# Kernel optimization log

Measured on AMD Instinct MI355X. Metric: run time of the kernel, lower is better.

Reference implementation:

```python
import jax, jax.numpy as jnp
import numpy as np

B, S, D, H = 2, 2048, 1024, 16
HD = D // H  # 64
NEG = 1.0e9


def setup_inputs() -> dict:
    key = jax.random.key(0)
    ks = jax.random.split(key, 9)
    scale = 1.0 / np.sqrt(D)
    return {
        "q_in": jax.random.normal(ks[0], (B, S, D), jnp.float32),
        "k_in": jax.random.normal(ks[1], (B, S, D), jnp.float32),
        "v_in": jax.random.normal(ks[2], (B, S, D), jnp.float32),
        "Wq": jax.random.normal(ks[3], (D, D), jnp.float32) * scale,
        "bq": jnp.zeros((D,), jnp.float32),
        "Wk": jax.random.normal(ks[4], (D, D), jnp.float32) * scale,
        "bk": jnp.zeros((D,), jnp.float32),
        "Wv": jax.random.normal(ks[5], (D, D), jnp.float32) * scale,
        "bv": jnp.zeros((D,), jnp.float32),
        "Wo": jax.random.normal(ks[6], (D, D), jnp.float32) * scale,
        "bo": jnp.zeros((D,), jnp.float32),
    }


def _split_heads(x):
    # [B,S,D] -> [B,H,S,HD]
    return x.reshape(B, S, H, HD).transpose(0, 2, 1, 3)


def reference(q_in, k_in, v_in, Wq, bq, Wk, bk, Wv, bv, Wo, bo):
    q = _split_heads(q_in @ Wq + bq)
    k = _split_heads(k_in @ Wk + bk)
    v = _split_heads(v_in @ Wv + bv)
    # scaled dot-product attention with additive causal mask (use_causal_mask=True)
    scores = jnp.einsum("bhqd,bhkd->bhqk", q, k) / jnp.sqrt(jnp.float32(HD))
    causal = jnp.tril(jnp.ones((S, S), jnp.float32))  # band_part(ones, -1, 0)
    scores = scores + (causal - 1.0) * NEG
    weights = jax.nn.softmax(scores, axis=-1)
    attn = jnp.einsum("bhqk,bhkd->bhqd", weights, v)
    concat = attn.transpose(0, 2, 1, 3).reshape(B, S, D)
    return concat @ Wo + bo
```

## Files before the change

kernel.cpp:

```cpp
#include <hip/hip_runtime.h>

#define B_  2
#define S_  2048
#define D_  1024
#define H_  16
#define HD_ 64
#define MM  (B_ * S_)

typedef __bf16 bf16;
typedef __attribute__((ext_vector_type(8))) __bf16 bf16x8;
typedef __attribute__((ext_vector_type(4))) __bf16 bf16x4;
typedef __attribute__((ext_vector_type(4))) float  f32x4;

__device__ inline float exp2g(float x) { return __builtin_amdgcn_exp2f(x); }

__device__ inline bf16x8 load8(const bf16* p) { return *(const bf16x8*)p; }
__device__ inline bf16x8 load8(const float* p) {
  float4 a = *(const float4*)p;
  float4 b = *(const float4*)(p + 4);
  bf16x8 r;
  r[0] = (bf16)a.x; r[1] = (bf16)a.y; r[2] = (bf16)a.z; r[3] = (bf16)a.w;
  r[4] = (bf16)b.x; r[5] = (bf16)b.y; r[6] = (bf16)b.z; r[7] = (bf16)b.w;
  return r;
}

__device__ inline void gld16(void* lds, const void* g) {
  __builtin_amdgcn_global_load_lds(
      (const __attribute__((address_space(1))) unsigned int*)g,
      (__attribute__((address_space(3))) unsigned int*)lds, 16, 0, 0);
}

__device__ inline void barrier_lds() {
  asm volatile("s_waitcnt lgkmcnt(0)" ::: "memory");
  __builtin_amdgcn_s_barrier();
}

__global__ __launch_bounds__(256) void transpose_w(
    const float* __restrict__ W0, const float* __restrict__ W1,
    const float* __restrict__ W2, const float* __restrict__ W3,
    bf16* __restrict__ T0, bf16* __restrict__ T1,
    bf16* __restrict__ T2, bf16* __restrict__ T3,
    const float* __restrict__ X0, const float* __restrict__ X1,
    const float* __restrict__ X2,
    bf16* __restrict__ Y0, bf16* __restrict__ Y1, bf16* __restrict__ Y2) {
  const int z = blockIdx.z;
  if (z >= 4) {
    const int p = z - 4, t = p >> 2;
    const float* src = t == 0 ? X0 : t == 1 ? X1 : X2;
    bf16* dst = t == 0 ? Y0 : t == 1 ? Y1 : Y2;
    long base = ((long)(p & 3) << 20) +
                (long)(blockIdx.y * 32 + blockIdx.x) * 1024 + threadIdx.x * 4;
    float4 v = *(const float4*)&src[base];
    bf16x4 o4;
    o4[0] = (bf16)v.x; o4[1] = (bf16)v.y; o4[2] = (bf16)v.z; o4[3] = (bf16)v.w;
    *(bf16x4*)&dst[base] = o4;
    return;
  }
  __shared__ bf16 t[32][40];
  const float* in = z == 0 ? W0 : z == 1 ? W1 : z == 2 ? W2 : W3;
  bf16* out = z == 0 ? T0 : z == 1 ? T1 : z == 2 ? T2 : T3;
  const int tx = threadIdx.x & 31;
  const int ty = threadIdx.x >> 5;
  const int r0 = blockIdx.y * 32, c0 = blockIdx.x * 32;
#pragma unroll
  for (int j = 0; j < 32; j += 8)
    t[ty + j][tx] = (bf16)in[(long)(r0 + ty + j) * D_ + (c0 + tx)];
  __syncthreads();
#pragma unroll
  for (int j = 0; j < 32; j += 8)
    out[(long)(c0 + ty + j) * D_ + (r0 + tx)] = t[tx][ty + j];
}

__global__ __launch_bounds__(256) void transpose_v64(const bf16* __restrict__ V,
                                                     bf16* __restrict__ VT) {
  __shared__ bf16 t[64][72];
  const int tid = threadIdx.x;
  const int s0 = blockIdx.x * 64;
  const int bh = blockIdx.y;
  const int b = bh >> 4, h = bh & 15;
  const bf16* ip = V + (long)b * S_ * D_ + h * HD_;
  bf16* op = VT + (long)bh * HD_ * S_;
#pragma unroll
  for (int i = 0; i < 2; ++i) {
    int c = tid + i * 256;
    int r = c >> 3, cc = (c & 7) * 8;
    *(bf16x8*)&t[r][cc] = *(const bf16x8*)&ip[(long)(s0 + r) * D_ + cc];
  }
  __syncthreads();
#pragma unroll
  for (int i = 0; i < 2; ++i) {
    int c = tid + i * 256;
    int d = c >> 3, sc = (c & 7) * 8;
    bf16x8 v;
#pragma unroll
    for (int j = 0; j < 8; ++j) v[j] = t[sc + j][d];
    *(bf16x8*)&op[(long)d * S_ + s0 + sc] = v;
  }
}

template <typename AT, typename OT>
__global__ __launch_bounds__(256) void gemm_bt_dma(
    const AT* __restrict__ A0, const AT* __restrict__ A1, const AT* __restrict__ A2,
    const bf16* __restrict__ B0, const bf16* __restrict__ B1, const bf16* __restrict__ B2,
    const float* __restrict__ c0, const float* __restrict__ c1, const float* __restrict__ c2,
    OT* __restrict__ C0, OT* __restrict__ C1, OT* __restrict__ C2,
    int M, int N, int K) {
  __shared__ bf16 lA[2][128][32];
  __shared__ bf16 lB[2][128][32];
  const int z = blockIdx.z;
  const AT*    A    = z == 0 ? A0 : z == 1 ? A1 : A2;
  const bf16*  Bt   = z == 0 ? B0 : z == 1 ? B1 : B2;
  const float* bias = z == 0 ? c0 : z == 1 ? c1 : c2;
  OT*          C    = z == 0 ? C0 : z == 1 ? C1 : C2;

  const int tid = threadIdx.x;
  const int lane = tid & 63, wave = tid >> 6;
  const int quad = lane >> 4, l16 = lane & 15;
  const int id = blockIdx.x + (blockIdx.y << 3);
  const int nid = (id & 7) * 32 + (id >> 3);
  const int bm = (nid >> 3) * 128, bn = (nid & 7) * 128;
  const int wm = (wave >> 1) * 64, wn = (wave & 1) * 64;

  f32x4 acc[4][4] = {};
  const int NT = K >> 5;

#define STAGE_DMA(buf, t)                                                    \
  {                                                                          \
    const int k0 = (t) << 5;                                                 \
    _Pragma("unroll") for (int i = 0; i < 2; ++i) {                          \
      const int nbase = wave * 128 + i * 64;    \
      const int n = nbase + lane;                                            \
      const int row = n >> 2, kc = (n & 3) * 8;                              \
      gld16(&lB[buf][0][0] + (long)nbase * 8,                                \
            &Bt[(long)(bn + row) * K + k0 + kc]);                            \
      if constexpr (__is_same(AT, bf16))                                     \
        gld16(&lA[buf][0][0] + (long)nbase * 8,                              \
              &A[(long)(bm + row) * K + k0 + kc]);                           \
    }                                                                        \
    if constexpr (!__is_same(AT, bf16)) {                                    \
      _Pragma("unroll") for (int i = 0; i < 2; ++i) {                        \
        int cch = tid + i * 256;                                             \
        int row = cch >> 2, kc = (cch & 3) * 8;                              \
        *(bf16x8*)&lA[buf][row][kc] =                                        \
            load8(&A[(long)(bm + row) * K + k0 + kc]);                       \
      }                                                                      \
    }                                                                        \
  }

  STAGE_DMA(0, 0);
  __syncthreads();

  for (int t = 0; t < NT; ++t) {
    const int buf = t & 1;
    if (t + 1 < NT) STAGE_DMA(buf ^ 1, t + 1);
    bf16x8 af[4], bfr[4];
#pragma unroll
    for (int i = 0; i < 4; ++i) {
      af[i]  = *(const bf16x8*)&lA[buf][wm + i * 16 + l16][quad * 8];
      bfr[i] = *(const bf16x8*)&lB[buf][wn + i * 16 + l16][quad * 8];
    }
#pragma unroll
    for (int mi = 0; mi < 4; ++mi)
#pragma unroll
      for (int ni = 0; ni < 4; ++ni)
        acc[mi][ni] = __builtin_amdgcn_mfma_f32_16x16x32_bf16(
            af[mi], bfr[ni], acc[mi][ni], 0, 0, 0);
    __syncthreads();
  }
#undef STAGE_DMA

#pragma unroll
  for (int mi = 0; mi < 4; ++mi)
#pragma unroll
    for (int ni = 0; ni < 4; ++ni) {
      int col = bn + wn + ni * 16 + l16;
      float bv = bias[col];
#pragma unroll
      for (int r = 0; r < 4; ++r) {
        int row = bm + wm + mi * 16 + quad * 4 + r;
        C[(long)row * N + col] = (OT)(acc[mi][ni][r] + bv);
      }
    }
}

__global__ __launch_bounds__(256) void gemm_bt_64(const bf16* __restrict__ A,
                                                  const bf16* __restrict__ Bt,
                                                  const float* __restrict__ bias,
                                                  float* __restrict__ C,
                                                  int M, int N, int K) {
  __shared__ bf16 lA[2][128][32];
  __shared__ bf16 lB[2][64][32];
  const int tid = threadIdx.x;
  const int lane = tid & 63, wave = tid >> 6;
  const int quad = lane >> 4, l16 = lane & 15;
  const int id = blockIdx.x + (blockIdx.y << 4);
  const int nid = (id & 7) * 64 + (id >> 3);
  const int bm = (nid >> 4) * 128, bn = (nid & 15) * 64;
  const int wm = (wave >> 1) * 64, wn = (wave & 1) * 32;

  f32x4 acc[4][2] = {};
  const int NT = K >> 5;

#define STAGE64(buf, t)                                                      \
  {                                                                          \
    const int k0 = (t) << 5;                                                 \
    _Pragma("unroll") for (int i = 0; i < 2; ++i) {                          \
      const int nbase = wave * 128 + i * 64;                                 \
      const int n = nbase + lane;                                            \
      const int row = n >> 2, kc = (n & 3) * 8;                              \
      gld16(&lA[buf][0][0] + (long)nbase * 8,                                \
            &A[(long)(bm + row) * K + k0 + kc]);                             \
    }                                                                        \
    {                                                                        \
      const int nbase = wave * 64;                                           \
      const int n = nbase + lane;                                            \
      const int row = n >> 2, kc = (n & 3) * 8;                              \
      gld16(&lB[buf][0][0] + (long)nbase * 8,                                \
            &Bt[(long)(bn + row) * K + k0 + kc]);                            \
    }                                                                        \
  }

  STAGE64(0, 0);
  __syncthreads();

  for (int t = 0; t < NT; ++t) {
    const int buf = t & 1;
    if (t + 1 < NT) STAGE64(buf ^ 1, t + 1);
    bf16x8 af[4], bfr[2];
#pragma unroll
    for (int i = 0; i < 4; ++i)
      af[i] = *(const bf16x8*)&lA[buf][wm + i * 16 + l16][quad * 8];
#pragma unroll
    for (int i = 0; i < 2; ++i)
      bfr[i] = *(const bf16x8*)&lB[buf][wn + i * 16 + l16][quad * 8];
#pragma unroll
    for (int mi = 0; mi < 4; ++mi)
#pragma unroll
      for (int ni = 0; ni < 2; ++ni)
        acc[mi][ni] = __builtin_amdgcn_mfma_f32_16x16x32_bf16(
            af[mi], bfr[ni], acc[mi][ni], 0, 0, 0);
    __syncthreads();
  }
#undef STAGE64

#pragma unroll
  for (int mi = 0; mi < 4; ++mi)
#pragma unroll
    for (int ni = 0; ni < 2; ++ni) {
      int col = bn + wn + ni * 16 + l16;
      float bv = bias[col];
#pragma unroll
      for (int r = 0; r < 4; ++r) {
        int row = bm + wm + mi * 16 + quad * 4 + r;
        C[(long)row * N + col] = acc[mi][ni][r] + bv;
      }
    }
}

#define SCALE_LOG2E 0.1803368801111244f

__device__ inline void attn_step5(bool diag, int qloc, int quad, int l16,
                                  const bf16 (*lKb)[64], const bf16 (*lVb)[64],
                                  bf16 (*lpw)[72], const bf16x8* aq,
                                  f32x4* o, float& l_s) {
  const int sw = l16 & 7;
  f32x4 s[4];
  __builtin_amdgcn_s_setprio(1);
#pragma unroll
  for (int ni = 0; ni < 4; ++ni) {
    f32x4 a = {};
#pragma unroll
    for (int c = 0; c < 2; ++c) {
      bf16x8 kf = *(const bf16x8*)&lKb[ni * 16 + l16][((c * 4 + quad) ^ sw) * 8];
      a = __builtin_amdgcn_mfma_f32_16x16x32_bf16(kf, aq[c], a, 0, 0, 0);
    }
    s[ni] = a * SCALE_LOG2E;
  }
  __builtin_amdgcn_s_setprio(0);
  if (diag) {
#pragma unroll
    for (int ni = 0; ni < 4; ++ni)
#pragma unroll
      for (int r = 0; r < 4; ++r)
        if (ni * 16 + quad * 4 + r > qloc) s[ni][r] = -1e9f;
  }
  float rs = 0.f;
#pragma unroll
  for (int ni = 0; ni < 4; ++ni) {
    bf16x4 p4;
#pragma unroll
    for (int r = 0; r < 4; ++r) {
      float p = exp2g(s[ni][r]);
      p4[r] = (bf16)p;
      rs += p;
    }
    *(bf16x4*)&lpw[l16][ni * 16 + quad * 4] = p4;
  }
  l_s += rs;
  __builtin_amdgcn_s_setprio(1);
#pragma unroll
  for (int c = 0; c < 2; ++c) {
    bf16x8 ap = *(const bf16x8*)&lpw[l16][c * 32 + quad * 8];
#pragma unroll
    for (int di = 0; di < 4; ++di) {
      bf16x8 vf = *(const bf16x8*)&lVb[di * 16 + l16][((c * 4 + quad) ^ sw) * 8];
      o[di] = __builtin_amdgcn_mfma_f32_16x16x32_bf16(vf, ap, o[di], 0, 0, 0);
    }
  }
  __builtin_amdgcn_s_setprio(0);
}

__device__ inline void store_o(bf16* Ob, int qrow, int lane, int quad, int l16,
                               bf16 (*lpw)[72], const f32x4* o, float l_s) {
  float rs = l_s;
  rs += __shfl_xor(rs, 16);
  rs += __shfl_xor(rs, 32);
  const float inv = 1.0f / rs;
#pragma unroll
  for (int di = 0; di < 4; ++di) {
    bf16x4 p4;
#pragma unroll
    for (int r = 0; r < 4; ++r) p4[r] = (bf16)(o[di][r] * inv);
    *(bf16x4*)&lpw[l16][di * 16 + quad * 4] = p4;
  }
  const int q = lane >> 2, db = (lane & 3) * 16;
  bf16x8 v0 = *(const bf16x8*)&lpw[q][db];
  bf16x8 v1 = *(const bf16x8*)&lpw[q][db + 8];
  *(bf16x8*)&Ob[(long)(qrow + q) * D_ + db] = v0;
  *(bf16x8*)&Ob[(long)(qrow + q) * D_ + db + 8] = v1;
}

__global__ __launch_bounds__(512) void flash_attn9(const bf16* __restrict__ Q,
                                                   const bf16* __restrict__ K,
                                                   const bf16* __restrict__ VT,
                                                   bf16* __restrict__ O) {
  __shared__ bf16 lK[2][64][64];
  __shared__ bf16 lV[2][64][64];
  __shared__ bf16 lp[8][16][72];
  const int tid = threadIdx.x;
  const int lane = tid & 63, wave = tid >> 6;
  const int quad = lane >> 4, l16 = lane & 15;
  const int x = blockIdx.x, bh = blockIdx.y;
  const bool flip = (bh & 16) != 0;
  const int qtA = flip ? 30 - 2 * x : 2 * x;
  const int qtB = qtA + 1;
  const bool isB = wave >= 4;
  const int w4 = wave & 3;
  const int myqt = isB ? qtB : qtA;
  const int b = bh >> 4, h = bh & 15;
  const bf16* Qb = Q + (long)b * S_ * D_ + h * HD_;
  const bf16* Kb = K + (long)b * S_ * D_ + h * HD_;
  const bf16* Vb = VT + (long)bh * HD_ * S_;
  const int qrow = myqt * 64 + w4 * 16;
  const int qloc = w4 * 16 + l16;

  bf16x8 aq[2];
#pragma unroll
  for (int c = 0; c < 2; ++c)
    aq[c] = *(const bf16x8*)&Qb[(long)(qrow + l16) * D_ + c * 32 + quad * 8];

  f32x4 o[4] = {};
  float l_s = 0.f;

  const int srow = tid >> 3, scol = tid & 7;
  const int swcol = (scol ^ (srow & 7)) * 8;
  const int ktMax = qtB;

  bf16x8 rkA, rvA, rkB, rvB;
  rkA = *(const bf16x8*)&Kb[(long)srow * D_ + scol * 8];
  rvA = *(const bf16x8*)&Vb[(long)srow * S_ + scol * 8];
  *(bf16x8*)&lK[0][srow][swcol] = rkA;
  *(bf16x8*)&lV[0][srow][swcol] = rvA;
  rkA = *(const bf16x8*)&Kb[(long)(64 + srow) * D_ + scol * 8];
  rvA = *(const bf16x8*)&Vb[(long)srow * S_ + 64 + scol * 8];
  barrier_lds();

  for (int kt = 0; kt < ktMax; kt += 2) {
    if (kt + 2 <= ktMax) {
      const long k0 = (long)(kt + 2) * 64;
      rkB = *(const bf16x8*)&Kb[(k0 + srow) * D_ + scol * 8];
      rvB = *(const bf16x8*)&Vb[(long)srow * S_ + k0 + scol * 8];
    }
    if (isB || kt <= qtA)
      attn_step5(kt == myqt, qloc, quad, l16, lK[0], lV[0], lp[wave], aq,
                 o, l_s);
    *(bf16x8*)&lK[1][srow][swcol] = rkA;
    *(bf16x8*)&lV[1][srow][swcol] = rvA;
    barrier_lds();
    if (kt + 3 <= ktMax) {
      const long k0 = (long)(kt + 3) * 64;
      rkA = *(const bf16x8*)&Kb[(k0 + srow) * D_ + scol * 8];
      rvA = *(const bf16x8*)&Vb[(long)srow * S_ + k0 + scol * 8];
    }
    if (isB || kt + 1 <= qtA)
      attn_step5(kt + 1 == myqt, qloc, quad, l16, lK[1], lV[1], lp[wave], aq,
                 o, l_s);
    if (kt + 1 < ktMax) {
      *(bf16x8*)&lK[0][srow][swcol] = rkB;
      *(bf16x8*)&lV[0][srow][swcol] = rvB;
      barrier_lds();
    }
  }

  bf16* Ob = O + (long)b * S_ * D_ + h * HD_;
  store_o(Ob, qrow, lane, quad, l16, lp[wave], o, l_s);
}

extern "C" void kernel_launch(void* const* d_in, const int* in_sizes, int n_in,
                              void* d_out, int out_size, void* d_ws, size_t ws_size,
                              hipStream_t stream) {
  (void)in_sizes; (void)n_in; (void)out_size;
  const float* q_in = (const float*)d_in[0];
  const float* k_in = (const float*)d_in[1];
  const float* v_in = (const float*)d_in[2];
  const float* Wq   = (const float*)d_in[3];
  const float* bq   = (const float*)d_in[4];
  const float* Wk   = (const float*)d_in[5];
  const float* bk   = (const float*)d_in[6];
  const float* Wv   = (const float*)d_in[7];
  const float* bv   = (const float*)d_in[8];
  const float* Wo   = (const float*)d_in[9];
  const float* bo   = (const float*)d_in[10];
  float* out = (float*)d_out;

  bf16* ws = (bf16*)d_ws;
  const size_t WSZ = (size_t)D_ * D_;
  const size_t TSZ = (size_t)B_ * S_ * D_;
  bf16* WqT = ws;
  bf16* WkT = WqT + WSZ;
  bf16* WvT = WkT + WSZ;
  bf16* WoT = WvT + WSZ;
  bf16* Qp  = WoT + WSZ;
  bf16* Kp  = Qp + TSZ;
  bf16* Vp  = Kp + TSZ;
  bf16* VTp = Vp + TSZ;
  bf16* Ap  = VTp + TSZ;
  bf16* Xq  = VTp;
  bf16* Xk  = Ap;
  bf16* Xv  = Ap + TSZ;
  const bool pre = ws_size >= (4 * WSZ + 6 * TSZ) * sizeof(bf16);

  dim3 blk(256);
  transpose_w<<<dim3(32, 32, pre ? 16 : 4), blk, 0, stream>>>(
      Wq, Wk, Wv, Wo, WqT, WkT, WvT, WoT, q_in, k_in, v_in, Xq, Xk, Xv);

  if (pre)
    gemm_bt_dma<bf16, bf16><<<dim3(8, 32, 3), blk, 0, stream>>>(
        Xq, Xk, Xv, WqT, WkT, WvT, bq, bk, bv, Qp, Kp, Vp, MM, D_, D_);
  else
    gemm_bt_dma<float, bf16><<<dim3(8, 32, 3), blk, 0, stream>>>(
        q_in, k_in, v_in, WqT, WkT, WvT, bq, bk, bv, Qp, Kp, Vp, MM, D_, D_);

  transpose_v64<<<dim3(S_ / 64, B_ * H_), blk, 0, stream>>>(Vp, VTp);

  flash_attn9<<<dim3(16, B_ * H_), dim3(512), 0, stream>>>(Qp, Kp, VTp, Ap);

  gemm_bt_64<<<dim3(16, 32), blk, 0, stream>>>(Ap, WoT, bo, out, MM, D_, D_);
}
```

Before: 211.1 us.

## Replace direct-to-LDS DMA with register-staged two-deep prefetch in GEMMs

Both projection GEMM kernels stop using global_load_lds. Each thread now loads its A/B slices into registers two k-tiles ahead, then writes them into the alternate LDS buffer after computing on the current one. The loop is unrolled by two, with one waitcnt+barrier per tile, so global load latency overlaps MFMA work more deeply. The trade is extra VGPRs for the staged tiles and explicit LDS store instructions in place of asynchronous DMA.

Result: slower. 220.5 us (+4.5%).

```diff
diff --git a/kernel.cpp b/kernel.cpp
--- a/kernel.cpp
+++ b/kernel.cpp
@@ -22,12 +22,6 @@
   r[0] = (bf16)a.x; r[1] = (bf16)a.y; r[2] = (bf16)a.z; r[3] = (bf16)a.w;
   r[4] = (bf16)b.x; r[5] = (bf16)b.y; r[6] = (bf16)b.z; r[7] = (bf16)b.w;
   return r;
-}
-
-__device__ inline void gld16(void* lds, const void* g) {
-  __builtin_amdgcn_global_load_lds(
-      (const __attribute__((address_space(1))) unsigned int*)g,
-      (__attribute__((address_space(3))) unsigned int*)lds, 16, 0, 0);
 }
 
 __device__ inline void barrier_lds() {
@@ -124,50 +118,59 @@
   f32x4 acc[4][4] = {};
   const int NT = K >> 5;
 
-#define STAGE_DMA(buf, t)                                                    \
+  const int srow = tid >> 2, skc = (tid & 3) * 8;
+
+#define LOADSET(ra0, ra1, rb0, rb1, t)                                       \
   {                                                                          \
     const int k0 = (t) << 5;                                                 \
-    _Pragma("unroll") for (int i = 0; i < 2; ++i) {                          \
-      const int nbase = wave * 128 + i * 64;    \
-      const int n = nbase + lane;                                            \
-      const int row = n >> 2, kc = (n & 3) * 8;                              \
-      gld16(&lB[buf][0][0] + (long)nbase * 8,                                \
-            &Bt[(long)(bn + row) * K + k0 + kc]);                            \
-      if constexpr (__is_same(AT, bf16))                                     \
-        gld16(&lA[buf][0][0] + (long)nbase * 8,                              \
-              &A[(long)(bm + row) * K + k0 + kc]);                           \
+    ra0 = load8(&A[(long)(bm + srow) * K + k0 + skc]);                       \
+    ra1 = load8(&A[(long)(bm + srow + 64) * K + k0 + skc]);                  \
+    rb0 = load8(&Bt[(long)(bn + srow) * K + k0 + skc]);                      \
+    rb1 = load8(&Bt[(long)(bn + srow + 64) * K + k0 + skc]);                 \
+  }
+#define WRITESET(buf, ra0, ra1, rb0, rb1)                                    \
+  {                                                                          \
+    *(bf16x8*)&lA[buf][srow][skc] = ra0;                                     \
+    *(bf16x8*)&lA[buf][srow + 64][skc] = ra1;                                \
+    *(bf16x8*)&lB[buf][srow][skc] = rb0;                                     \
+    *(bf16x8*)&lB[buf][srow + 64][skc] = rb1;                                \
+  }
+#define COMPUTE(buf)                                                         \
+  {                                                                          \
+    bf16x8 af[4], bfr[4];                                                    \
+    _Pragma("unroll") for (int i = 0; i < 4; ++i) {                          \
+      af[i]  = *(const bf16x8*)&lA[buf][wm + i * 16 + l16][quad * 8];        \
+      bfr[i] = *(const bf16x8*)&lB[buf][wn + i * 16 + l16][quad * 8];        \
     }                                                                        \
-    if constexpr (!__is_same(AT, bf16)) {                                    \
-      _Pragma("unroll") for (int i = 0; i < 2; ++i) {                        \
-        int cch = tid + i * 256;                                             \
-        int row = cch >> 2, kc = (cch & 3) * 8;                              \
-        *(bf16x8*)&lA[buf][row][kc] =                                        \
-            load8(&A[(long)(bm + row) * K + k0 + kc]);                       \
-      }                                                                      \
-    }                                                                        \
-  }
-
-  STAGE_DMA(0, 0);
-  __syncthreads();
-
-  for (int t = 0; t < NT; ++t) {
-    const int buf = t & 1;
-    if (t + 1 < NT) STAGE_DMA(buf ^ 1, t + 1);
-    bf16x8 af[4], bfr[4];
-#pragma unroll
-    for (int i = 0; i < 4; ++i) {
-      af[i]  = *(const bf16x8*)&lA[buf][wm + i * 16 + l16][quad * 8];
-      bfr[i] = *(const bf16x8*)&lB[buf][wn + i * 16 + l16][quad * 8];
-    }
-#pragma unroll
-    for (int mi = 0; mi < 4; ++mi)
-#pragma unroll
-      for (int ni = 0; ni < 4; ++ni)
-        acc[mi][ni] = __builtin_amdgcn_mfma_f32_16x16x32_bf16(
-            af[mi], bfr[ni], acc[mi][ni], 0, 0, 0);
-    __syncthreads();
-  }
-#undef STAGE_DMA
+    _Pragma("unroll") for (int mi = 0; mi < 4; ++mi)                         \
+      _Pragma("unroll") for (int ni = 0; ni < 4; ++ni)                       \
+        acc[mi][ni] = __builtin_amdgcn_mfma_f32_16x16x32_bf16(               \
+            af[mi], bfr[ni], acc[mi][ni], 0, 0, 0);                          \
+  }
+
+  bf16x8 a0, a1, b0, b1;
+  bf16x8 a2, a3, b2, b3;
+
+  LOADSET(a0, a1, b0, b1, 0);
+  WRITESET(0, a0, a1, b0, b1);
+  LOADSET(a0, a1, b0, b1, 1);
+  barrier_lds();
+
+  for (int kt = 0; kt < NT; kt += 2) {
+    if (kt + 2 < NT) LOADSET(a2, a3, b2, b3, kt + 2);
+    COMPUTE(0);
+    WRITESET(1, a0, a1, b0, b1);
+    barrier_lds();
+    if (kt + 3 < NT) LOADSET(a0, a1, b0, b1, kt + 3);
+    COMPUTE(1);
+    if (kt + 2 < NT) {
+      WRITESET(0, a2, a3, b2, b3);
+      barrier_lds();
+    }
+  }
+#undef LOADSET
+#undef WRITESET
+#undef COMPUTE
 
 #pragma unroll
   for (int mi = 0; mi < 4; ++mi)
@@ -201,47 +204,57 @@
   f32x4 acc[4][2] = {};
   const int NT = K >> 5;
 
-#define STAGE64(buf, t)                                                      \
+  const int srow = tid >> 2, skc = (tid & 3) * 8;
+
+#define LOADSET64(ra0, ra1, rb0, t)                                          \
   {                                                                          \
     const int k0 = (t) << 5;                                                 \
-    _Pragma("unroll") for (int i = 0; i < 2; ++i) {                          \
-      const int nbase = wave * 128 + i * 64;                                 \
-      const int n = nbase + lane;                                            \
-      const int row = n >> 2, kc = (n & 3) * 8;                              \
-      gld16(&lA[buf][0][0] + (long)nbase * 8,                                \
-            &A[(long)(bm + row) * K + k0 + kc]);                             \
-    }                                                                        \
-    {                                                                        \
-      const int nbase = wave * 64;                                           \
-      const int n = nbase + lane;                                            \
-      const int row = n >> 2, kc = (n & 3) * 8;                              \
-      gld16(&lB[buf][0][0] + (long)nbase * 8,                                \
-            &Bt[(long)(bn + row) * K + k0 + kc]);                            \
-    }                                                                        \
-  }
-
-  STAGE64(0, 0);
-  __syncthreads();
-
-  for (int t = 0; t < NT; ++t) {
-    const int buf = t & 1;
-    if (t + 1 < NT) STAGE64(buf ^ 1, t + 1);
-    bf16x8 af[4], bfr[2];
-#pragma unroll
-    for (int i = 0; i < 4; ++i)
-      af[i] = *(const bf16x8*)&lA[buf][wm + i * 16 + l16][quad * 8];
-#pragma unroll
-    for (int i = 0; i < 2; ++i)
-      bfr[i] = *(const bf16x8*)&lB[buf][wn + i * 16 + l16][quad * 8];
-#pragma unroll
-    for (int mi = 0; mi < 4; ++mi)
-#pragma unroll
-      for (int ni = 0; ni < 2; ++ni)
-        acc[mi][ni] = __builtin_amdgcn_mfma_f32_16x16x32_bf16(
-            af[mi], bfr[ni], acc[mi][ni], 0, 0, 0);
-    __syncthreads();
-  }
-#undef STAGE64
+    ra0 = load8(&A[(long)(bm + srow) * K + k0 + skc]);                       \
+    ra1 = load8(&A[(long)(bm + srow + 64) * K + k0 + skc]);                  \
+    rb0 = load8(&Bt[(long)(bn + srow) * K + k0 + skc]);                      \
+  }
+#define WRITESET64(buf, ra0, ra1, rb0)                                       \
+  {                                                                          \
+    *(bf16x8*)&lA[buf][srow][skc] = ra0;                                     \
+    *(bf16x8*)&lA[buf][srow + 64][skc] = ra1;                                \
+    *(bf16x8*)&lB[buf][srow][skc] = rb0;                                     \
+  }
+#define COMPUTE64(buf)                                                       \
+  {                                                                          \
+    bf16x8 af[4], bfr[2];                                                    \
+    _Pragma("unroll") for (int i = 0; i < 4; ++i)                            \
+      af[i] = *(const bf16x8*)&lA[buf][wm + i * 16 + l16][quad * 8];         \
+    _Pragma("unroll") for (int i = 0; i < 2; ++i)                            \
+      bfr[i] = *(const bf16x8*)&lB[buf][wn + i * 16 + l16][quad * 8];        \
+    _Pragma("unroll") for (int mi = 0; mi < 4; ++mi)                         \
+      _Pragma("unroll") for (int ni = 0; ni < 2; ++ni)                       \
+        acc[mi][ni] = __builtin_amdgcn_mfma_f32_16x16x32_bf16(               \
+            af[mi], bfr[ni], acc[mi][ni], 0, 0, 0);                          \
+  }
+
+  bf16x8 a0, a1, b0;
+  bf16x8 a2, a3, b2;
+
+  LOADSET64(a0, a1, b0, 0);
+  WRITESET64(0, a0, a1, b0);
+  LOADSET64(a0, a1, b0, 1);
+  barrier_lds();
+
+  for (int kt = 0; kt < NT; kt += 2) {
+    if (kt + 2 < NT) LOADSET64(a2, a3, b2, kt + 2);
+    COMPUTE64(0);
+    WRITESET64(1, a0, a1, b0);
+    barrier_lds();
+    if (kt + 3 < NT) LOADSET64(a0, a1, b0, kt + 3);
+    COMPUTE64(1);
+    if (kt + 2 < NT) {
+      WRITESET64(0, a2, a3, b2);
+      barrier_lds();
+    }
+  }
+#undef LOADSET64
+#undef WRITESET64
+#undef COMPUTE64
 
 #pragma unroll
   for (int mi = 0; mi < 4; ++mi)
```
